# Optimization experiments

Measured on AMD Instinct MI355X. Metric: run time of the kernel, lower is better.

The kernel has to match this reference:

```python
import jax, jax.numpy as jnp
import numpy as np

B, S, D = 4, 4096, 1024
GROUP = 256
HEAD = 128
INNER = 2048


def setup_inputs() -> dict:
    key = jax.random.key(0)
    ks = jax.random.split(key, 16)
    s = 0.02
    return {
        'x': jax.random.normal(ks[0], (B, S, D), jnp.float32),
        'Wv': jax.random.normal(ks[1], (D, INNER), jnp.float32) * s,
        'bv': jnp.zeros((INNER,), jnp.float32),
        'Wg': jax.random.normal(ks[2], (D, INNER), jnp.float32) * s,
        'bg': jnp.zeros((INNER,), jnp.float32),
        'Win': jax.random.normal(ks[3], (D, HEAD), jnp.float32) * s,
        'bin_': jnp.zeros((HEAD,), jnp.float32),
        'Wout': jax.random.normal(ks[4], (INNER, D), jnp.float32) * s,
        'bout': jnp.zeros((D,), jnp.float32),
        'g_qq': 1.0 + jax.random.normal(ks[5], (HEAD,), jnp.float32) * s,
        'b_qq': jnp.zeros((HEAD,), jnp.float32),
        'g_qk': 1.0 + jax.random.normal(ks[6], (HEAD,), jnp.float32) * s,
        'b_qk': jnp.zeros((HEAD,), jnp.float32),
        'g_lq': 1.0 + jax.random.normal(ks[7], (HEAD,), jnp.float32) * s,
        'b_lq': jnp.zeros((HEAD,), jnp.float32),
        'g_lk': 1.0 + jax.random.normal(ks[8], (HEAD,), jnp.float32) * s,
        'b_lk': jnp.zeros((HEAD,), jnp.float32),
    }


def reference(x, Wv, bv, Wg, bg, Win, bin_, Wout, bout,
              g_qq, b_qq, g_qk, b_qk, g_lq, b_lq, g_lk, b_lk):
    b, s, d = x.shape
    g = s // GROUP
    xc = x.reshape(b, g, GROUP, d)                       # [B,G,C,D]
    v = jax.nn.silu(xc @ Wv + bv)                        # [B,G,C,E]
    gate = jax.nn.silu(xc @ Wg + bg)                     # [B,G,C,E]
    x_ = jax.nn.silu(xc @ Win + bin_)                    # [B,G,C,H]
    quad_q = x_ * g_qq + b_qq
    quad_k = x_ * g_qk + b_qk
    lin_q = x_ * g_lq + b_lq
    lin_k = x_ * g_lk + b_lk
    # local quadratic relu^2 attention per chunk
    scale = jnp.asarray(INNER ** 0.5, x.dtype)           # v.size(-1)**0.5
    attn = jnp.einsum('bgns,bgms->bgnm', quad_q, quad_k) / scale
    causal_mask = jnp.triu(jnp.ones((GROUP, GROUP), bool), 1)
    attn = jnp.where(causal_mask, 0.0, attn)
    attn = jnp.square(jax.nn.relu(attn))
    v_quad = jnp.einsum('bgnm,bgme->bgne', attn, v)
    # global causal linear attention: exclusive cumsum of per-chunk k^T v over chunks
    kv = jnp.einsum('bgcs,bgce->bgse', lin_k, v)         # [B,G,H,E]
    kv = jnp.cumsum(kv, axis=1) - kv                     # exclusive over chunk dim
    v_lin = jnp.einsum('bgcs,bgse->bgce', lin_q, kv)
    o = (v_quad + v_lin) * gate
    o = o @ Wout + bout
    return o.reshape(b, s, d)
```

## Files before the change

### kernel.cpp

```cpp
#include <hip/hip_runtime.h>

typedef __attribute__((ext_vector_type(8))) short short8;
typedef __attribute__((ext_vector_type(4))) float floatx4;
typedef __attribute__((ext_vector_type(4))) unsigned short ushort4v;
typedef unsigned short u16;

#define DEV __device__ __forceinline__

DEV u16 f2bf(float f) {
  unsigned int u = __float_as_uint(f);
  u += 0x7fffu + ((u >> 16) & 1u);
  return (u16)(u >> 16);
}
DEV float bf2f(u16 h) { return __uint_as_float(((unsigned int)h) << 16); }
DEV float silu_f(float x) { return x / (1.f + __expf(-x)); }
DEV floatx4 fzero() { floatx4 z = {0.f, 0.f, 0.f, 0.f}; return z; }
DEV floatx4 mfma16(short8 a, short8 b, floatx4 c) {
  return __builtin_amdgcn_mfma_f32_16x16x32_bf16(a, b, c, 0, 0, 0);
}
DEV void gll16(const void* g, void* l) {
  __builtin_amdgcn_global_load_lds((__attribute__((address_space(1))) void*)g,
                                   (__attribute__((address_space(3))) void*)l,
                                   16, 0, 0);
}

__global__ __launch_bounds__(256) void cast_x_kernel(const float* __restrict__ x,
                                                     u16* __restrict__ xb, int n4) {
  int i = blockIdx.x * 256 + threadIdx.x;
  if (i >= n4) return;
  float4 v = ((const float4*)x)[i];
  ushort4v o;
  o[0] = f2bf(v.x); o[1] = f2bf(v.y); o[2] = f2bf(v.z); o[3] = f2bf(v.w);
  *(ushort4v*)&xb[(size_t)i * 4] = o;
}

__global__ __launch_bounds__(256) void transpose_cast_kernel(const float* __restrict__ W,
                                                             u16* __restrict__ WT,
                                                             int K, int N) {
  __shared__ u16 tile[32][36];
  int n0 = blockIdx.x * 32, k0 = blockIdx.y * 32;
  int t = threadIdx.x;
  int r = t >> 3, cs = (t & 7) * 4;
  float4 v = *(const float4*)&W[(size_t)(k0 + r) * N + n0 + cs];
  tile[r][cs + 0] = f2bf(v.x);
  tile[r][cs + 1] = f2bf(v.y);
  tile[r][cs + 2] = f2bf(v.z);
  tile[r][cs + 3] = f2bf(v.w);
  __syncthreads();
  ushort4v o;
  o[0] = tile[cs + 0][r];
  o[1] = tile[cs + 1][r];
  o[2] = tile[cs + 2][r];
  o[3] = tile[cs + 3][r];
  *(ushort4v*)&WT[(size_t)(n0 + r) * K + k0 + cs] = o;
}

DEV void wave_transposed_store(u16* __restrict__ Ct, long chunk_stride,
                               const u16* trw, int chunk, int cbase, int nbase,
                               int lane) {
#pragma unroll
  for (int it = 0; it < 8; ++it) {
    int e_l = it * 8 + (lane >> 3);
    int c_off = (lane & 7) * 8;
    short8 val = *(const short8*)&trw[e_l * 72 + c_off];
    *(short8*)&Ct[(size_t)chunk * chunk_stride + (size_t)(nbase + e_l) * 256 + cbase +
                  c_off] = val;
  }
}

template <int MODE>
__global__ __launch_bounds__(256) void gemm_bt(
    const u16* __restrict__ A, const u16* __restrict__ Bt, int M, int N, int K,
    int nshift, const float* __restrict__ bias, u16* __restrict__ Cn,
    float* __restrict__ Cf, u16* __restrict__ Ct, long ct_stride,
    u16* __restrict__ Cn2, u16* __restrict__ Cn3,
    const float* __restrict__ gqq, const float* __restrict__ bqq,
    const float* __restrict__ gqk, const float* __restrict__ bqk,
    const float* __restrict__ glq, const float* __restrict__ blq,
    const float* __restrict__ glk, const float* __restrict__ blk) {
  __shared__ union {
    struct { u16 a[128 * 64]; u16 b[128 * 64]; } st;
    u16 tr[4 * 64 * 72];
  } sm;
  const int t = threadIdx.x;
  const int wave = t >> 6, lane = t & 63;
  const int l15 = lane & 15, l16 = lane >> 4;
  const int ell = blockIdx.x;
  const int xcd = ell & 7, i = ell >> 3;
  const int mtiles_per_xcd = M >> 10;
  const int m0 = (xcd * mtiles_per_xcd + (i >> nshift)) * 128;
  const int n0 = (i & ((1 << nshift) - 1)) * 128;
  const int wm = (wave >> 1) * 64, wn = (wave & 1) * 64;

  floatx4 acc[4][4];
#pragma unroll
  for (int i2 = 0; i2 < 4; ++i2)
#pragma unroll
    for (int j = 0; j < 4; ++j) acc[i2][j] = fzero();

  const u16* pa[4];
  const u16* pb[4];
#pragma unroll
  for (int j = 0; j < 4; ++j) {
    const int c = t + 256 * j;
    const int r = c >> 3, p = c & 7;
    const int g = p ^ (r & 7);
    pa[j] = A + (size_t)(m0 + r) * K + g * 8;
    pb[j] = Bt + (size_t)(n0 + r) * K + g * 8;
  }

  for (int k0 = 0; k0 < K; k0 += 64) {
    __syncthreads();
#pragma unroll
    for (int j = 0; j < 4; ++j) {
      gll16(pa[j] + k0, &sm.st.a[(t + 256 * j) * 8]);
      gll16(pb[j] + k0, &sm.st.b[(t + 256 * j) * 8]);
    }
    __syncthreads();
#pragma unroll
    for (int s = 0; s < 2; ++s) {
      short8 af[4], bfr[4];
#pragma unroll
      for (int mi = 0; mi < 4; ++mi) {
        const int wr = wm + mi * 16 + l15;
        af[mi] = *(const short8*)&sm.st.a[wr * 64 + ((s * 4 + l16) ^ (wr & 7)) * 8];
      }
#pragma unroll
      for (int ni = 0; ni < 4; ++ni) {
        const int wr = wn + ni * 16 + l15;
        bfr[ni] = *(const short8*)&sm.st.b[wr * 64 + ((s * 4 + l16) ^ (wr & 7)) * 8];
      }
#pragma unroll
      for (int mi = 0; mi < 4; ++mi)
#pragma unroll
        for (int ni = 0; ni < 4; ++ni)
          acc[mi][ni] = mfma16(af[mi], bfr[ni], acc[mi][ni]);
    }
  }
  __syncthreads();

  if constexpr (MODE == 0) {
    u16* trw = &sm.tr[wave * 64 * 72];
#pragma unroll
    for (int mi = 0; mi < 4; ++mi)
#pragma unroll
      for (int ni = 0; ni < 4; ++ni) {
        const int col = n0 + wn + ni * 16 + l15;
        const float bc = bias[col];
#pragma unroll
        for (int r = 0; r < 4; ++r)
          trw[(mi * 16 + l16 * 4 + r) * 72 + ni * 16 + l15] =
              f2bf(silu_f(acc[mi][ni][r] + bc));
      }
#pragma unroll
    for (int it = 0; it < 8; ++it) {
      const int m_l = it * 8 + (lane >> 3);
      const int n_off = (lane & 7) * 8;
      *(short8*)&Cn[(size_t)(m0 + wm + m_l) * N + n0 + wn + n_off] =
          *(const short8*)&trw[m_l * 72 + n_off];
    }
  } else if constexpr (MODE == 3) {
#pragma unroll
    for (int mi = 0; mi < 4; ++mi)
#pragma unroll
      for (int ni = 0; ni < 4; ++ni) {
        const int col = n0 + wn + ni * 16 + l15;
        const float bc = bias[col];
        const int row = m0 + wm + mi * 16 + l16 * 4;
#pragma unroll
        for (int r = 0; r < 4; ++r)
          Cf[(size_t)(row + r) * N + col] = acc[mi][ni][r] + bc;
      }
  } else if constexpr (MODE == 1) {
    u16* trw = &sm.tr[wave * 64 * 72];
#pragma unroll
    for (int mi = 0; mi < 4; ++mi)
#pragma unroll
      for (int ni = 0; ni < 4; ++ni) {
        const int col = n0 + wn + ni * 16 + l15;
        const float bc = bias[col];
        ushort4v p;
#pragma unroll
        for (int r = 0; r < 4; ++r) p[r] = f2bf(silu_f(acc[mi][ni][r] + bc));
        *(ushort4v*)&trw[(ni * 16 + l15) * 72 + mi * 16 + l16 * 4] = p;
      }
    wave_transposed_store(Ct, ct_stride, trw, (m0 + wm) >> 8, (m0 + wm) & 255,
                          n0 + wn, lane);
  } else {
    u16* trw = &sm.tr[wave * 64 * 72];
#pragma unroll
    for (int mi = 0; mi < 4; ++mi)
#pragma unroll
      for (int ni = 0; ni < 4; ++ni) {
        const int col = wn + ni * 16 + l15;
        const float bc = bias[col];
        const float Gqq = gqq[col], Bqq = bqq[col];
        const float Gqk = gqk[col], Bqk = bqk[col];
        const float Glq = glq[col], Blq = blq[col];
        const float Glk = glk[col], Blk = blk[col];
        const int row = m0 + wm + mi * 16 + l16 * 4;
        ushort4v p;
#pragma unroll
        for (int r = 0; r < 4; ++r) {
          const float sv = silu_f(acc[mi][ni][r] + bc);
          const size_t ad = (size_t)(row + r) * N + col;
          Cn[ad] = f2bf(sv * Gqq + Bqq);
          Cn2[ad] = f2bf(sv * Gqk + Bqk);
          Cn3[ad] = f2bf(sv * Glq + Blq);
          p[r] = f2bf(sv * Glk + Blk);
        }
        *(ushort4v*)&trw[(ni * 16 + l15) * 72 + mi * 16 + l16 * 4] = p;
      }
    wave_transposed_store(Ct, ct_stride, trw, (m0 + wm) >> 8, (m0 + wm) & 255, wn,
                          lane);
  }
}

__global__ __launch_bounds__(256) void kv_kernel(const u16* __restrict__ vT,
                                                 const u16* __restrict__ lkT,
                                                 u16* __restrict__ kv) {
  const int chunk = blockIdx.y;
  const int et = blockIdx.x;
  const int w = threadIdx.x >> 6, lane = threadIdx.x & 63;
  const int l15 = lane & 15, l16 = lane >> 4;
  const size_t vb = (size_t)chunk * (2048 * 256) + (size_t)et * (128 * 256);
  const size_t lb = (size_t)chunk * (128 * 256);
  const int we = (w >> 1) * 64, wh = (w & 1) * 64;
  floatx4 acc[4][4];
#pragma unroll
  for (int i = 0; i < 4; ++i)
#pragma unroll
    for (int j = 0; j < 4; ++j) acc[i][j] = fzero();
  for (int kk = 0; kk < 8; ++kk) {
    short8 av[4], bv[4];
#pragma unroll
    for (int mi = 0; mi < 4; ++mi)
      av[mi] = *(const short8*)&vT[vb + (size_t)(we + mi * 16 + l15) * 256 + kk * 32 +
                                   l16 * 8];
#pragma unroll
    for (int ni = 0; ni < 4; ++ni)
      bv[ni] = *(const short8*)&lkT[lb + (size_t)(wh + ni * 16 + l15) * 256 + kk * 32 +
                                    l16 * 8];
#pragma unroll
    for (int mi = 0; mi < 4; ++mi)
#pragma unroll
      for (int ni = 0; ni < 4; ++ni) acc[mi][ni] = mfma16(av[mi], bv[ni], acc[mi][ni]);
  }
  u16* out = kv + (size_t)chunk * (2048 * 128);
#pragma unroll
  for (int mi = 0; mi < 4; ++mi)
#pragma unroll
    for (int ni = 0; ni < 4; ++ni) {
      const int h = wh + ni * 16 + l15;
      const int e = et * 128 + we + mi * 16 + l16 * 4;
#pragma unroll
      for (int r = 0; r < 4; ++r) out[(size_t)(e + r) * 128 + h] = f2bf(acc[mi][ni][r]);
    }
}

__global__ __launch_bounds__(256) void cumsum_kernel(u16* __restrict__ kv) {
  const int idx = blockIdx.x * 256 + threadIdx.x;
  const int b = blockIdx.y;
  float s = 0.f;
  for (int g = 0; g < 16; ++g) {
    const size_t a = (size_t)(b * 16 + g) * 262144 + idx;
    const float v = bf2f(kv[a]);
    kv[a] = f2bf(s);
    s += v;
  }
}

__global__ __launch_bounds__(256) void attn_kernel(
    const u16* __restrict__ qq, const u16* __restrict__ qk, const u16* __restrict__ lq,
    const u16* __restrict__ vT, const u16* __restrict__ kvT,
    u16* __restrict__ gate_op) {
  __shared__ u16 S[64][264];
  const int chunk = blockIdx.y;
  const int e0 = blockIdx.x * 256;
  const int tok0 = chunk * 256;
  const int w = threadIdx.x >> 6, lane = threadIdx.x & 63;
  const int l15 = lane & 15, l16 = lane >> 4;
  const float isc = 0.022097086912079608f;
  const size_t vbase = (size_t)chunk * (2048 * 256);
  const size_t kbase = (size_t)chunk * (2048 * 128);
  const int ew = e0 + w * 64;

  for (int ns = 0; ns < 4; ++ns) {
    const int r0 = ns * 64 + w * 16;
    short8 af[4];
#pragma unroll
    for (int kk = 0; kk < 4; ++kk)
      af[kk] = *(const short8*)&qq[(size_t)(tok0 + r0 + l15) * 128 + kk * 32 + l16 * 8];
    const int mt_cnt = (r0 >> 4) + 1;
    const int mt_all = (ns + 1) * 4;
    const int srow = w * 16 + l16 * 4;
    for (int mt = 0; mt < mt_all; ++mt) {
      if (mt < mt_cnt) {
        floatx4 a = fzero();
#pragma unroll
        for (int kk = 0; kk < 4; ++kk) {
          short8 bq =
              *(const short8*)&qk[(size_t)(tok0 + mt * 16 + l15) * 128 + kk * 32 +
                                  l16 * 8];
          a = mfma16(af[kk], bq, a);
        }
        const int mcol = mt * 16 + l15;
#pragma unroll
        for (int r = 0; r < 4; ++r) {
          const int nrow = r0 + l16 * 4 + r;
          float sv = a[r] * isc;
          sv = (mcol <= nrow) ? sv : 0.f;
          sv = fmaxf(sv, 0.f);
          S[srow + r][mcol] = f2bf(sv * sv);
        }
      } else {
#pragma unroll
        for (int r = 0; r < 4; ++r) S[srow + r][mt * 16 + l15] = (u16)0;
      }
    }
    __syncthreads();

    floatx4 acc[4][4];
#pragma unroll
    for (int i = 0; i < 4; ++i)
#pragma unroll
      for (int j = 0; j < 4; ++j) acc[i][j] = fzero();

    const int ks = (ns + 1) * 2;
    for (int kk = 0; kk < ks; ++kk) {
      short8 sa[4];
#pragma unroll
      for (int nt = 0; nt < 4; ++nt)
        sa[nt] = *(const short8*)&S[nt * 16 + l15][kk * 32 + l16 * 8];
#pragma unroll
      for (int ei = 0; ei < 4; ++ei) {
        short8 vb = *(const short8*)&vT[vbase + (size_t)(ew + ei * 16 + l15) * 256 +
                                        kk * 32 + l16 * 8];
#pragma unroll
        for (int nt = 0; nt < 4; ++nt) acc[nt][ei] = mfma16(sa[nt], vb, acc[nt][ei]);
      }
    }
#pragma unroll
    for (int kk = 0; kk < 4; ++kk) {
      short8 la[4];
#pragma unroll
      for (int nt = 0; nt < 4; ++nt)
        la[nt] = *(const short8*)&lq[(size_t)(tok0 + ns * 64 + nt * 16 + l15) * 128 +
                                     kk * 32 + l16 * 8];
#pragma unroll
      for (int ei = 0; ei < 4; ++ei) {
        short8 kb = *(const short8*)&kvT[kbase + (size_t)(ew + ei * 16 + l15) * 128 +
                                         kk * 32 + l16 * 8];
#pragma unroll
        for (int nt = 0; nt < 4; ++nt) acc[nt][ei] = mfma16(la[nt], kb, acc[nt][ei]);
      }
    }
#pragma unroll
    for (int nt = 0; nt < 4; ++nt)
#pragma unroll
      for (int ei = 0; ei < 4; ++ei) {
        const int e_g = ew + ei * 16 + l15;
        const int nb = tok0 + ns * 64 + nt * 16 + l16 * 4;
#pragma unroll
        for (int r = 0; r < 4; ++r) {
          const size_t ad = (size_t)(nb + r) * 2048 + e_g;
          const float gv = bf2f(gate_op[ad]);
          gate_op[ad] = f2bf(acc[nt][ei][r] * gv);
        }
      }
    __syncthreads();
  }
}

extern "C" void kernel_launch(void* const* d_in, const int* in_sizes, int n_in,
                              void* d_out, int out_size, void* d_ws, size_t ws_size,
                              hipStream_t stream) {
  (void)in_sizes; (void)n_in; (void)out_size; (void)ws_size;
  const float* x = (const float*)d_in[0];
  const float* Wv = (const float*)d_in[1];
  const float* bv = (const float*)d_in[2];
  const float* Wg = (const float*)d_in[3];
  const float* bg = (const float*)d_in[4];
  const float* Win = (const float*)d_in[5];
  const float* bin = (const float*)d_in[6];
  const float* Wout = (const float*)d_in[7];
  const float* bout = (const float*)d_in[8];
  const float* gqq = (const float*)d_in[9];
  const float* bqq = (const float*)d_in[10];
  const float* gqk = (const float*)d_in[11];
  const float* bqk = (const float*)d_in[12];
  const float* glq = (const float*)d_in[13];
  const float* blq = (const float*)d_in[14];
  const float* glk = (const float*)d_in[15];
  const float* blk = (const float*)d_in[16];

  char* p = (char*)d_ws;
  u16* xb = (u16*)p;   p += (size_t)16384 * 1024 * 2;
  u16* wvT = (u16*)p;  p += (size_t)2048 * 1024 * 2;
  u16* wgT = (u16*)p;  p += (size_t)2048 * 1024 * 2;
  u16* winT = (u16*)p; p += (size_t)128 * 1024 * 2;
  u16* woT = (u16*)p;  p += (size_t)1024 * 2048 * 2;
  u16* vTb = (u16*)p;  p += (size_t)64 * 2048 * 256 * 2;
  u16* gate = (u16*)p; p += (size_t)16384 * 2048 * 2;
  u16* qqb = (u16*)p;  p += (size_t)16384 * 128 * 2;
  u16* qkb = (u16*)p;  p += (size_t)16384 * 128 * 2;
  u16* lqb = (u16*)p;  p += (size_t)16384 * 128 * 2;
  u16* lkTb = (u16*)p; p += (size_t)64 * 128 * 256 * 2;
  u16* kvb = (u16*)p;  p += (size_t)64 * 2048 * 128 * 2;

  cast_x_kernel<<<16384, 256, 0, stream>>>(x, xb, 4194304);
  transpose_cast_kernel<<<dim3(64, 32), 256, 0, stream>>>(Wv, wvT, 1024, 2048);
  transpose_cast_kernel<<<dim3(64, 32), 256, 0, stream>>>(Wg, wgT, 1024, 2048);
  transpose_cast_kernel<<<dim3(4, 32), 256, 0, stream>>>(Win, winT, 1024, 128);
  transpose_cast_kernel<<<dim3(32, 64), 256, 0, stream>>>(Wout, woT, 2048, 1024);

  gemm_bt<1><<<2048, 256, 0, stream>>>(
      xb, wvT, 16384, 2048, 1024, 4, bv, nullptr, nullptr, vTb, 2048L * 256, nullptr,
      nullptr, nullptr, nullptr, nullptr, nullptr, nullptr, nullptr, nullptr, nullptr);
  gemm_bt<0><<<2048, 256, 0, stream>>>(
      xb, wgT, 16384, 2048, 1024, 4, bg, gate, nullptr, nullptr, 0, nullptr, nullptr,
      nullptr, nullptr, nullptr, nullptr, nullptr, nullptr, nullptr, nullptr);
  gemm_bt<2><<<128, 256, 0, stream>>>(
      xb, winT, 16384, 128, 1024, 0, bin, qqb, nullptr, lkTb, 128L * 256, qkb, lqb,
      gqq, bqq, gqk, bqk, glq, blq, glk, blk);

  kv_kernel<<<dim3(16, 64), 256, 0, stream>>>(vTb, lkTb, kvb);
  cumsum_kernel<<<dim3(1024, 4), 256, 0, stream>>>(kvb);
  attn_kernel<<<dim3(8, 64), 256, 0, stream>>>(qqb, qkb, lqb, vTb, kvb, gate);

  gemm_bt<3><<<1024, 256, 0, stream>>>(
      gate, woT, 16384, 1024, 2048, 3, bout, nullptr, (float*)d_out, nullptr, 0,
      nullptr, nullptr, nullptr, nullptr, nullptr, nullptr, nullptr, nullptr, nullptr,
      nullptr);
}
```

Measured before the change: 601.6 us.

## Fuse V and gate projection GEMMs into one kernel sharing A tiles

```diff
diff --git a/kernel.cpp b/kernel.cpp
--- a/kernel.cpp
+++ b/kernel.cpp
@@ -65,6 +65,110 @@
     short8 val = *(const short8*)&trw[e_l * 72 + c_off];
     *(short8*)&Ct[(size_t)chunk * chunk_stride + (size_t)(nbase + e_l) * 256 + cbase +
                   c_off] = val;
+  }
+}
+
+__global__ __launch_bounds__(256, 2) void gemm_vg(
+    const u16* __restrict__ A, const u16* __restrict__ Bv, const u16* __restrict__ Bg,
+    const float* __restrict__ bvb, const float* __restrict__ bgb,
+    u16* __restrict__ vT, u16* __restrict__ gate) {
+  constexpr int K = 1024, N = 2048;
+  __shared__ union {
+    struct { u16 a[128 * 64]; u16 b[2][128 * 64]; } st;
+    u16 tr[4 * 64 * 72];
+  } sm;
+  const int t = threadIdx.x;
+  const int wave = t >> 6, lane = t & 63;
+  const int l15 = lane & 15, l16 = lane >> 4;
+  const int ell = blockIdx.x;
+  const int xcd = ell & 7, i = ell >> 3;
+  const int m0 = (xcd * 16 + (i >> 4)) * 128;
+  const int n0 = (i & 15) * 128;
+  const int wm = (wave >> 1) * 64, wn = (wave & 1) * 64;
+
+  floatx4 accv[4][4], accg[4][4];
+#pragma unroll
+  for (int a = 0; a < 4; ++a)
+#pragma unroll
+    for (int b = 0; b < 4; ++b) { accv[a][b] = fzero(); accg[a][b] = fzero(); }
+
+  const u16 *pa[4], *pbv[4], *pbg[4];
+#pragma unroll
+  for (int j = 0; j < 4; ++j) {
+    const int c = t + 256 * j;
+    const int r = c >> 3, p = c & 7;
+    const int g = p ^ (r & 7);
+    const size_t off = (size_t)r * K + g * 8;
+    pa[j] = A + (size_t)m0 * K + off;
+    pbv[j] = Bv + (size_t)n0 * K + off;
+    pbg[j] = Bg + (size_t)n0 * K + off;
+  }
+
+  for (int k0 = 0; k0 < K; k0 += 64) {
+    __syncthreads();
+#pragma unroll
+    for (int j = 0; j < 4; ++j) {
+      const int d = (t + 256 * j) * 8;
+      gll16(pa[j] + k0, &sm.st.a[d]);
+      gll16(pbv[j] + k0, &sm.st.b[0][d]);
+      gll16(pbg[j] + k0, &sm.st.b[1][d]);
+    }
+    __syncthreads();
+#pragma unroll
+    for (int s = 0; s < 2; ++s) {
+      short8 af[4], b0[4], b1[4];
+#pragma unroll
+      for (int mi = 0; mi < 4; ++mi) {
+        const int wr = wm + mi * 16 + l15;
+        af[mi] = *(const short8*)&sm.st.a[wr * 64 + ((s * 4 + l16) ^ (wr & 7)) * 8];
+      }
+#pragma unroll
+      for (int ni = 0; ni < 4; ++ni) {
+        const int wr = wn + ni * 16 + l15;
+        const int sl = wr * 64 + ((s * 4 + l16) ^ (wr & 7)) * 8;
+        b0[ni] = *(const short8*)&sm.st.b[0][sl];
+        b1[ni] = *(const short8*)&sm.st.b[1][sl];
+      }
+#pragma unroll
+      for (int mi = 0; mi < 4; ++mi)
+#pragma unroll
+        for (int ni = 0; ni < 4; ++ni) {
+          accv[mi][ni] = mfma16(af[mi], b0[ni], accv[mi][ni]);
+          accg[mi][ni] = mfma16(af[mi], b1[ni], accg[mi][ni]);
+        }
+    }
+  }
+  __syncthreads();
+
+  u16* trw = &sm.tr[wave * 64 * 72];
+#pragma unroll
+  for (int mi = 0; mi < 4; ++mi)
+#pragma unroll
+    for (int ni = 0; ni < 4; ++ni) {
+      const float bc = bvb[n0 + wn + ni * 16 + l15];
+      ushort4v p;
+#pragma unroll
+      for (int r = 0; r < 4; ++r) p[r] = f2bf(silu_f(accv[mi][ni][r] + bc));
+      *(ushort4v*)&trw[(ni * 16 + l15) * 72 + mi * 16 + l16 * 4] = p;
+    }
+  wave_transposed_store(vT, 2048L * 256, trw, (m0 + wm) >> 8, (m0 + wm) & 255,
+                        n0 + wn, lane);
+#pragma unroll
+  for (int mi = 0; mi < 4; ++mi)
+#pragma unroll
+    for (int ni = 0; ni < 4; ++ni) {
+      const float bc = bgb[n0 + wn + ni * 16 + l15];
+#pragma unroll
+      for (int r = 0; r < 4; ++r)
+        trw[(mi * 16 + l16 * 4 + r) * 72 + ni * 16 + l15] =
+            f2bf(silu_f(accg[mi][ni][r] + bc));
+    }
+#pragma unroll
+  for (int it = 0; it < 8; ++it) {
+    const int m_l = it * 8 + (lane >> 3);
+    const int n_off = (lane & 7) * 8;
+    *(short8*)&gate[(size_t)(m0 + wm + m_l) * N + n0 + wn + n_off] =
+        *(const short8*)&trw[m_l * 72 + n_off];
   }
 }
 
@@ -139,27 +243,7 @@
   }
   __syncthreads();
 
-  if constexpr (MODE == 0) {
-    u16* trw = &sm.tr[wave * 64 * 72];
-#pragma unroll
-    for (int mi = 0; mi < 4; ++mi)
-#pragma unroll
-      for (int ni = 0; ni < 4; ++ni) {
-        const int col = n0 + wn + ni * 16 + l15;
-        const float bc = bias[col];
-#pragma unroll
-        for (int r = 0; r < 4; ++r)
-          trw[(mi * 16 + l16 * 4 + r) * 72 + ni * 16 + l15] =
-              f2bf(silu_f(acc[mi][ni][r] + bc));
-      }
-#pragma unroll
-    for (int it = 0; it < 8; ++it) {
-      const int m_l = it * 8 + (lane >> 3);
-      const int n_off = (lane & 7) * 8;
-      *(short8*)&Cn[(size_t)(m0 + wm + m_l) * N + n0 + wn + n_off] =
-          *(const short8*)&trw[m_l * 72 + n_off];
-    }
-  } else if constexpr (MODE == 3) {
+  if constexpr (MODE == 3) {
 #pragma unroll
     for (int mi = 0; mi < 4; ++mi)
 #pragma unroll
@@ -171,21 +255,6 @@
         for (int r = 0; r < 4; ++r)
           Cf[(size_t)(row + r) * N + col] = acc[mi][ni][r] + bc;
       }
-  } else if constexpr (MODE == 1) {
-    u16* trw = &sm.tr[wave * 64 * 72];
-#pragma unroll
-    for (int mi = 0; mi < 4; ++mi)
-#pragma unroll
-      for (int ni = 0; ni < 4; ++ni) {
-        const int col = n0 + wn + ni * 16 + l15;
-        const float bc = bias[col];
-        ushort4v p;
-#pragma unroll
-        for (int r = 0; r < 4; ++r) p[r] = f2bf(silu_f(acc[mi][ni][r] + bc));
-        *(ushort4v*)&trw[(ni * 16 + l15) * 72 + mi * 16 + l16 * 4] = p;
-      }
-    wave_transposed_store(Ct, ct_stride, trw, (m0 + wm) >> 8, (m0 + wm) & 255,
-                          n0 + wn, lane);
   } else {
     u16* trw = &sm.tr[wave * 64 * 72];
 #pragma unroll
@@ -414,12 +483,7 @@
   transpose_cast_kernel<<<dim3(4, 32), 256, 0, stream>>>(Win, winT, 1024, 128);
   transpose_cast_kernel<<<dim3(32, 64), 256, 0, stream>>>(Wout, woT, 2048, 1024);
 
-  gemm_bt<1><<<2048, 256, 0, stream>>>(
-      xb, wvT, 16384, 2048, 1024, 4, bv, nullptr, nullptr, vTb, 2048L * 256, nullptr,
-      nullptr, nullptr, nullptr, nullptr, nullptr, nullptr, nullptr, nullptr, nullptr);
-  gemm_bt<0><<<2048, 256, 0, stream>>>(
-      xb, wgT, 16384, 2048, 1024, 4, bg, gate, nullptr, nullptr, 0, nullptr, nullptr,
-      nullptr, nullptr, nullptr, nullptr, nullptr, nullptr, nullptr, nullptr);
+  gemm_vg<<<2048, 256, 0, stream>>>(xb, wvT, wgT, bv, bg, vTb, gate);
   gemm_bt<2><<<128, 256, 0, stream>>>(
       xb, winT, 16384, 128, 1024, 0, bin, qqb, nullptr, lkTb, 128L * 256, qkb, lqb,
       gqq, bqq, gqk, bqk, glq, blq, glk, blk);
```

Measured after the change: 559.7 us. -7.0%, faster.
